# Kernel optimization log

Measured on AMD Instinct MI355X. Metric: run time of the kernel, lower is better.

## Reference

```python
import jax, jax.numpy as jnp
import numpy as np

N = 50000   # nodes
E = 800000  # edges (avg degree 16)
D = 96      # input feature dim
U = 96      # units (== D, so no dense_i projection)


def _glorot(key, fan_in, fan_out):
    limit = np.sqrt(6.0 / (fan_in + fan_out)).astype(np.float32)
    return jax.random.uniform(key, (fan_in, fan_out), jnp.float32, -limit, limit)


def setup_inputs() -> dict:
    key = jax.random.key(0)
    ks = jax.random.split(key, 8)
    X = jax.random.normal(ks[0], (N, D), jnp.float32)
    row = jax.random.randint(ks[1], (E,), 0, N, jnp.int32)   # destination nodes
    col = jax.random.randint(ks[2], (E,), 0, N, jnp.int32)   # source nodes
    a_vals = jax.random.uniform(ks[3], (E,), jnp.float32)    # adjacency values
    return {
        "X": X,
        "a_vals": a_vals,
        "Wn": _glorot(ks[4], D, U), "bn": jnp.zeros((U,), jnp.float32),
        "Wgi": _glorot(ks[5], D, U), "bgi": jnp.zeros((U,), jnp.float32),
        "Wgn": _glorot(ks[6], U, U), "bgn": jnp.zeros((U,), jnp.float32),
        "row": row, "col": col,
    }


def reference(X, a_vals, Wn, bn, Wgi, bgi, Wgn, bgn, row, col):
    # new_X = dense_n(X); new_X = A @ new_X  (SpMM via gather + segment_sum)
    newX = X @ Wn + bn                       # [N, U]
    msgs = a_vals[:, None] * newX[col]       # [E, U]
    agg = jax.ops.segment_sum(msgs, row, num_segments=N)  # [N, U]
    # gate = sigmoid(dense_gate_i(X) + dense_gate_n(agg))
    gate = jax.nn.sigmoid(X @ Wgi + bgi + agg @ Wgn + bgn)
    # units == inp_dim -> no dense_i; gated residual combine
    return agg * gate + X * (1.0 - gate)
```

## Files before the change

### kernel.cpp

```cpp
#include <hip/hip_runtime.h>
#include <math.h>


#define DU 96
#define DU4 24
#define NSUB 64
#define NGRP 8
#define HMAX 6656

typedef unsigned int uint;
typedef unsigned short ushort;
typedef __attribute__((ext_vector_type(8))) short short8;
typedef __attribute__((ext_vector_type(4))) float f32x4;

__device__ inline uint bf16r(float x) {
  uint u = __float_as_uint(x);
  return (u + 0x7FFFu + ((u >> 16) & 1u)) >> 16;
}

__global__ __launch_bounds__(256) void k_fuse1(
    const float* __restrict__ X, const float* __restrict__ Wn,
    const float* __restrict__ bn, const float* __restrict__ Wgi,
    const float* __restrict__ Wgn, const int* __restrict__ row,
    ushort* __restrict__ Xb, ushort* __restrict__ newXb,
    ushort* __restrict__ WTgi, ushort* __restrict__ WTgn,
    int* __restrict__ pc, int N, int E, int ntile) {
  __shared__ __align__(16) char smem[31744];
  ushort* WL = (ushort*)smem;
  typedef ushort XsRow[104];
  XsRow* Xs = (XsRow*)(smem + 18432);
  const int tid = threadIdx.x;
  const int lane = tid & 63, w = tid >> 6;
  const int m = lane & 15, q = lane >> 4;

  if ((int)blockIdx.x < ntile) {
    if (blockIdx.x == 0) {
      for (int i = tid; i < DU * DU; i += 256) {
        int n = i / DU, k = i % DU;
        WTgi[i] = (ushort)bf16r(Wgi[k * DU + n]);
      }
    } else if (blockIdx.x == 1) {
      for (int i = tid; i < DU * DU; i += 256) {
        int n = i / DU, k = i % DU;
        WTgn[i] = (ushort)bf16r(Wgn[k * DU + n]);
      }
    }
    for (int idx = tid; idx < 9216; idx += 256) {
      int j = idx & 7, ln = (idx >> 3) & 63, tk = idx >> 9;
      int ks = tk / 6, t = tk % 6;
      int k = ks * 32 + (ln >> 4) * 8 + j;
      int n = t * 16 + (ln & 15);
      WL[idx] = (ushort)bf16r(Wn[k * DU + n]);
    }
    const int row0 = blockIdx.x * 64;
    for (int i = tid; i < 64 * 48; i += 256) {
      int r = i / 48, cu = i % 48;
      int gr = row0 + r;
      uint packed = 0;
      if (gr < N) {
        float2 v = ((const float2*)X)[(size_t)gr * 48 + cu];
        packed = bf16r(v.x) | (bf16r(v.y) << 16);
        ((uint*)Xb)[(size_t)gr * 48 + cu] = packed;
      }
      *(uint*)&Xs[r][cu * 2] = packed;
    }
    __syncthreads();

    f32x4 acc[6];
#pragma unroll
    for (int t = 0; t < 6; ++t) acc[t] = (f32x4){0.f, 0.f, 0.f, 0.f};
#pragma unroll
    for (int ks = 0; ks < 3; ++ks) {
      short8 af = *(const short8*)&Xs[w * 16 + m][ks * 32 + q * 8];
#pragma unroll
      for (int t = 0; t < 6; ++t) {
        short8 bf = *(const short8*)&WL[((ks * 6 + t) * 64 + lane) * 8];
        acc[t] = __builtin_amdgcn_mfma_f32_16x16x32_bf16(af, bf, acc[t], 0, 0, 0);
      }
    }
    __syncthreads();
#pragma unroll
    for (int t = 0; t < 6; ++t) {
      int c = t * 16 + m;
      float bb = bn[c];
#pragma unroll
      for (int i = 0; i < 4; ++i)
        Xs[w * 16 + q * 4 + i][c] = (ushort)bf16r(acc[t][i] + bb);
    }
    __syncthreads();
    for (int i = tid; i < 64 * 48; i += 256) {
      int r = i / 48, cu = i % 48;
      int gr = row0 + r;
      if (gr < N) ((uint*)newXb)[(size_t)gr * 48 + cu] = *(uint*)&Xs[r][cu * 2];
    }
  } else {
    int* hist = (int*)smem;
    const int hb = (int)blockIdx.x - ntile;
    const int g = (int)(blockIdx.x & 7);
    const int sub = hb >> 3;
    const int d0 = (int)((long long)N * g >> 3);
    const int d1 = (int)((long long)N * (g + 1) >> 3);
    const int hs = d1 - d0;
    for (int j = tid; j < hs; j += 256) hist[j] = 0;
    __syncthreads();
    const int e0 = (int)(((long long)E * sub) >> 6);
    const int e1 = (int)(((long long)E * (sub + 1)) >> 6);
    int i = e0 + tid;
    for (; i + 768 < e1; i += 1024) {
      int a0 = row[i], a1 = row[i + 256], a2 = row[i + 512], a3 = row[i + 768];
      if (a0 >= d0 && a0 < d1) atomicAdd(&hist[a0 - d0], 1);
      if (a1 >= d0 && a1 < d1) atomicAdd(&hist[a1 - d0], 1);
      if (a2 >= d0 && a2 < d1) atomicAdd(&hist[a2 - d0], 1);
      if (a3 >= d0 && a3 < d1) atomicAdd(&hist[a3 - d0], 1);
    }
    for (; i < e1; i += 256) {
      int d = row[i];
      if (d >= d0 && d < d1) atomicAdd(&hist[d - d0], 1);
    }
    __syncthreads();
    for (int j = tid; j < hs; j += 256) pc[(size_t)sub * N + d0 + j] = hist[j];
  }
}

__global__ __launch_bounds__(256) void k_colsum(const int* __restrict__ pc,
                                                int* __restrict__ psub, int N) {
  int d = blockIdx.x * 256 + threadIdx.x;
  if (d >= N) return;
  int run = 0;
#pragma unroll 8
  for (int s = 0; s < NSUB; ++s) {
    int v = pc[(size_t)s * N + d];
    psub[(size_t)s * N + d] = run;
    run += v;
  }
}

__global__ __launch_bounds__(1024) void k_scan(const int* __restrict__ pc,
                                               const int* __restrict__ psub,
                                               int* __restrict__ off, int N) {
  __shared__ int ws[16];
  __shared__ int carry_s;
  const int* pcL = pc + (size_t)(NSUB - 1) * N;
  const int* psL = psub + (size_t)(NSUB - 1) * N;
  const int tid = threadIdx.x;
  const int lane = tid & 63, wid = tid >> 6;
  if (tid == 0) carry_s = 0;
  __syncthreads();
  const int PT = 8;
  const int CH = 1024 * PT;
  for (int base = 0; base < N; base += CH) {
    int idx = base + tid * PT;
    int tot[PT];
    int s = 0;
    if (idx < N) {
      int4 a0 = ((const int4*)(pcL + idx))[0];
      int4 a1 = ((const int4*)(pcL + idx))[1];
      int4 b0 = ((const int4*)(psL + idx))[0];
      int4 b1 = ((const int4*)(psL + idx))[1];
      tot[0] = a0.x + b0.x; tot[1] = a0.y + b0.y;
      tot[2] = a0.z + b0.z; tot[3] = a0.w + b0.w;
      tot[4] = a1.x + b1.x; tot[5] = a1.y + b1.y;
      tot[6] = a1.z + b1.z; tot[7] = a1.w + b1.w;
#pragma unroll
      for (int j = 0; j < PT; ++j) s += tot[j];
    } else {
#pragma unroll
      for (int j = 0; j < PT; ++j) tot[j] = 0;
    }
    int incl = s;
#pragma unroll
    for (int d = 1; d < 64; d <<= 1) {
      int t = __shfl_up(incl, d, 64);
      if (lane >= d) incl += t;
    }
    if (lane == 63) ws[wid] = incl;
    __syncthreads();
    int carry = carry_s;
    int wexcl = 0;
#pragma unroll
    for (int k = 0; k < 16; ++k)
      if (k < wid) wexcl += ws[k];
    int running = carry + wexcl + (incl - s);
    if (idx < N) {
      int4 o1, o2;
      o1.x = running; running += tot[0];
      o1.y = running; running += tot[1];
      o1.z = running; running += tot[2];
      o1.w = running; running += tot[3];
      o2.x = running; running += tot[4];
      o2.y = running; running += tot[5];
      o2.z = running; running += tot[6];
      o2.w = running; running += tot[7];
      ((int4*)(off + idx))[0] = o1;
      ((int4*)(off + idx))[1] = o2;
    }
    __syncthreads();
    if (tid == 0) {
      int t16 = 0;
#pragma unroll
      for (int k = 0; k < 16; ++k) t16 += ws[k];
      carry_s += t16;
    }
    __syncthreads();
  }
  if (tid == 0) off[N] = carry_s;
}

__global__ __launch_bounds__(256) void k_scatter(const int* __restrict__ row,
                                                 const int* __restrict__ col,
                                                 const float* __restrict__ a_vals,
                                                 const int* __restrict__ off,
                                                 const int* __restrict__ psub,
                                                 int2* __restrict__ ec,
                                                 int N, int E) {
  __shared__ int cur[HMAX];
  const int g = (int)(blockIdx.x & 7);
  const int sub = (int)(blockIdx.x >> 3);
  const int d0 = (int)((long long)N * g >> 3);
  const int d1 = (int)((long long)N * (g + 1) >> 3);
  const int hs = d1 - d0;
  for (int j = threadIdx.x; j < hs; j += 256)
    cur[j] = off[d0 + j] + psub[(size_t)sub * N + d0 + j];
  __syncthreads();
  const int e0 = (int)(((long long)E * sub) >> 6);
  const int e1 = (int)(((long long)E * (sub + 1)) >> 6);
  int i = e0 + (int)threadIdx.x;
  for (; i + 768 < e1; i += 1024) {
    int a0 = row[i], a1 = row[i + 256], a2 = row[i + 512], a3 = row[i + 768];
    if (a0 >= d0 && a0 < d1) {
      int s = atomicAdd(&cur[a0 - d0], 1);
      ec[s] = make_int2(col[i], __float_as_int(a_vals[i]));
    }
    if (a1 >= d0 && a1 < d1) {
      int s = atomicAdd(&cur[a1 - d0], 1);
      ec[s] = make_int2(col[i + 256], __float_as_int(a_vals[i + 256]));
    }
    if (a2 >= d0 && a2 < d1) {
      int s = atomicAdd(&cur[a2 - d0], 1);
      ec[s] = make_int2(col[i + 512], __float_as_int(a_vals[i + 512]));
    }
    if (a3 >= d0 && a3 < d1) {
      int s = atomicAdd(&cur[a3 - d0], 1);
      ec[s] = make_int2(col[i + 768], __float_as_int(a_vals[i + 768]));
    }
  }
  for (; i < e1; i += 256) {
    int d = row[i];
    if (d >= d0 && d < d1) {
      int s = atomicAdd(&cur[d - d0], 1);
      ec[s] = make_int2(col[i], __float_as_int(a_vals[i]));
    }
  }
}

__global__ __launch_bounds__(256) void k_agg(const ushort* __restrict__ newXb,
                                             const int* __restrict__ off,
                                             const int2* __restrict__ ec,
                                             ushort* __restrict__ aggb, int N) {
  int i = blockIdx.x * 256 + threadIdx.x;
  int r = i / 12;
  int c = i % 12;
  if (r >= N) return;
  int o0 = off[r];
  int e1 = off[r + 1] - o0;
  const int2* ep = ec + o0;
  float accA[8], accB[8];
#pragma unroll
  for (int k = 0; k < 8; ++k) { accA[k] = 0.f; accB[k] = 0.f; }
  int e = 0;
  for (; e + 4 <= e1; e += 4) {
    int2 p0 = ep[e + 0];
    int2 p1 = ep[e + 1];
    int2 p2 = ep[e + 2];
    int2 p3 = ep[e + 3];
    uint4 v0 = *(const uint4*)(newXb + (size_t)p0.x * DU + c * 8);
    uint4 v1 = *(const uint4*)(newXb + (size_t)p1.x * DU + c * 8);
    uint4 v2 = *(const uint4*)(newXb + (size_t)p2.x * DU + c * 8);
    uint4 v3 = *(const uint4*)(newXb + (size_t)p3.x * DU + c * 8);
    float a0 = __int_as_float(p0.y), a1 = __int_as_float(p1.y);
    float a2 = __int_as_float(p2.y), a3 = __int_as_float(p3.y);
    accA[0] = fmaf(a0, __uint_as_float(v0.x << 16), accA[0]);
    accA[1] = fmaf(a0, __uint_as_float(v0.x & 0xFFFF0000u), accA[1]);
    accA[2] = fmaf(a0, __uint_as_float(v0.y << 16), accA[2]);
    accA[3] = fmaf(a0, __uint_as_float(v0.y & 0xFFFF0000u), accA[3]);
    accA[4] = fmaf(a0, __uint_as_float(v0.z << 16), accA[4]);
    accA[5] = fmaf(a0, __uint_as_float(v0.z & 0xFFFF0000u), accA[5]);
    accA[6] = fmaf(a0, __uint_as_float(v0.w << 16), accA[6]);
    accA[7] = fmaf(a0, __uint_as_float(v0.w & 0xFFFF0000u), accA[7]);
    accB[0] = fmaf(a1, __uint_as_float(v1.x << 16), accB[0]);
    accB[1] = fmaf(a1, __uint_as_float(v1.x & 0xFFFF0000u), accB[1]);
    accB[2] = fmaf(a1, __uint_as_float(v1.y << 16), accB[2]);
    accB[3] = fmaf(a1, __uint_as_float(v1.y & 0xFFFF0000u), accB[3]);
    accB[4] = fmaf(a1, __uint_as_float(v1.z << 16), accB[4]);
    accB[5] = fmaf(a1, __uint_as_float(v1.z & 0xFFFF0000u), accB[5]);
    accB[6] = fmaf(a1, __uint_as_float(v1.w << 16), accB[6]);
    accB[7] = fmaf(a1, __uint_as_float(v1.w & 0xFFFF0000u), accB[7]);
    accA[0] = fmaf(a2, __uint_as_float(v2.x << 16), accA[0]);
    accA[1] = fmaf(a2, __uint_as_float(v2.x & 0xFFFF0000u), accA[1]);
    accA[2] = fmaf(a2, __uint_as_float(v2.y << 16), accA[2]);
    accA[3] = fmaf(a2, __uint_as_float(v2.y & 0xFFFF0000u), accA[3]);
    accA[4] = fmaf(a2, __uint_as_float(v2.z << 16), accA[4]);
    accA[5] = fmaf(a2, __uint_as_float(v2.z & 0xFFFF0000u), accA[5]);
    accA[6] = fmaf(a2, __uint_as_float(v2.w << 16), accA[6]);
    accA[7] = fmaf(a2, __uint_as_float(v2.w & 0xFFFF0000u), accA[7]);
    accB[0] = fmaf(a3, __uint_as_float(v3.x << 16), accB[0]);
    accB[1] = fmaf(a3, __uint_as_float(v3.x & 0xFFFF0000u), accB[1]);
    accB[2] = fmaf(a3, __uint_as_float(v3.y << 16), accB[2]);
    accB[3] = fmaf(a3, __uint_as_float(v3.y & 0xFFFF0000u), accB[3]);
    accB[4] = fmaf(a3, __uint_as_float(v3.z << 16), accB[4]);
    accB[5] = fmaf(a3, __uint_as_float(v3.z & 0xFFFF0000u), accB[5]);
    accB[6] = fmaf(a3, __uint_as_float(v3.w << 16), accB[6]);
    accB[7] = fmaf(a3, __uint_as_float(v3.w & 0xFFFF0000u), accB[7]);
  }
  for (; e < e1; ++e) {
    int2 p = ep[e];
    uint4 v = *(const uint4*)(newXb + (size_t)p.x * DU + c * 8);
    float a = __int_as_float(p.y);
    accA[0] = fmaf(a, __uint_as_float(v.x << 16), accA[0]);
    accA[1] = fmaf(a, __uint_as_float(v.x & 0xFFFF0000u), accA[1]);
    accA[2] = fmaf(a, __uint_as_float(v.y << 16), accA[2]);
    accA[3] = fmaf(a, __uint_as_float(v.y & 0xFFFF0000u), accA[3]);
    accA[4] = fmaf(a, __uint_as_float(v.z << 16), accA[4]);
    accA[5] = fmaf(a, __uint_as_float(v.z & 0xFFFF0000u), accA[5]);
    accA[6] = fmaf(a, __uint_as_float(v.w << 16), accA[6]);
    accA[7] = fmaf(a, __uint_as_float(v.w & 0xFFFF0000u), accA[7]);
  }
#pragma unroll
  for (int k = 0; k < 8; ++k) accA[k] += accB[k];
  uint4 o;
  o.x = bf16r(accA[0]) | (bf16r(accA[1]) << 16);
  o.y = bf16r(accA[2]) | (bf16r(accA[3]) << 16);
  o.z = bf16r(accA[4]) | (bf16r(accA[5]) << 16);
  o.w = bf16r(accA[6]) | (bf16r(accA[7]) << 16);
  *(uint4*)(aggb + (size_t)r * DU + c * 8) = o;
}

__global__ __launch_bounds__(256) void k_gateM(const ushort* __restrict__ Xb,
                                               const ushort* __restrict__ aggb,
                                               const ushort* __restrict__ WTgi,
                                               const ushort* __restrict__ WTgn,
                                               const float* __restrict__ bgi,
                                               const float* __restrict__ bgn,
                                               const float* __restrict__ X,
                                               float* __restrict__ Out, int N) {
  __shared__ float Gs[64][100];
  const int tid = threadIdx.x;
  const int lane = tid & 63, w = tid >> 6;
  const int m = lane & 15, q = lane >> 4;
  const int row0 = blockIdx.x * 64;
  int ar = row0 + w * 16 + m;
  if (ar > N - 1) ar = N - 1;

  f32x4 acc[6];
#pragma unroll
  for (int t = 0; t < 6; ++t) acc[t] = (f32x4){0.f, 0.f, 0.f, 0.f};

#pragma unroll
  for (int ks = 0; ks < 3; ++ks) {
    short8 af = *(const short8*)(Xb + (size_t)ar * DU + ks * 32 + q * 8);
#pragma unroll
    for (int t = 0; t < 6; ++t) {
      short8 bf = *(const short8*)(WTgi + (size_t)(t * 16 + m) * DU + ks * 32 + q * 8);
      acc[t] = __builtin_amdgcn_mfma_f32_16x16x32_bf16(af, bf, acc[t], 0, 0, 0);
    }
  }
#pragma unroll
  for (int ks = 0; ks < 3; ++ks) {
    short8 af = *(const short8*)(aggb + (size_t)ar * DU + ks * 32 + q * 8);
#pragma unroll
    for (int t = 0; t < 6; ++t) {
      short8 bf = *(const short8*)(WTgn + (size_t)(t * 16 + m) * DU + ks * 32 + q * 8);
      acc[t] = __builtin_amdgcn_mfma_f32_16x16x32_bf16(af, bf, acc[t], 0, 0, 0);
    }
  }

#pragma unroll
  for (int t = 0; t < 6; ++t) {
    int c = t * 16 + m;
    float bb = bgi[c] + bgn[c];
#pragma unroll
    for (int i = 0; i < 4; ++i) {
      float z = acc[t][i] + bb;
      Gs[w * 16 + q * 4 + i][c] = 1.f / (1.f + __expf(-z));
    }
  }
  __syncthreads();

  for (int j = tid; j < 64 * DU4; j += 256) {
    int r = j / DU4, c = j % DU4;
    int gr = row0 + r;
    if (gr < N) {
      float4 xv = ((const float4*)X)[(size_t)gr * DU4 + c];
      uint2 av = ((const uint2*)aggb)[(size_t)gr * DU4 + c];
      float a0 = __uint_as_float(av.x << 16);
      float a1 = __uint_as_float(av.x & 0xFFFF0000u);
      float a2 = __uint_as_float(av.y << 16);
      float a3 = __uint_as_float(av.y & 0xFFFF0000u);
      const float* gp = &Gs[r][c * 4];
      float4 o;
      o.x = xv.x + gp[0] * (a0 - xv.x);
      o.y = xv.y + gp[1] * (a1 - xv.y);
      o.z = xv.z + gp[2] * (a2 - xv.z);
      o.w = xv.w + gp[3] * (a3 - xv.w);
      ((float4*)Out)[(size_t)gr * DU4 + c] = o;
    }
  }
}

extern "C" void kernel_launch(void* const* d_in, const int* in_sizes, int n_in,
                              void* d_out, int out_size, void* d_ws, size_t ws_size,
                              hipStream_t stream) {
  const float* X      = (const float*)d_in[0];
  const float* a_vals = (const float*)d_in[1];
  const float* Wn     = (const float*)d_in[2];
  const float* bn     = (const float*)d_in[3];
  const float* Wgi    = (const float*)d_in[4];
  const float* bgi    = (const float*)d_in[5];
  const float* Wgn    = (const float*)d_in[6];
  const float* bgn    = (const float*)d_in[7];
  const int*   row    = (const int*)d_in[8];
  const int*   col    = (const int*)d_in[9];
  float* out = (float*)d_out;

  const int N = in_sizes[0] / DU;
  const int E = in_sizes[1];
  const int ntile = (N + 63) / 64;
  const int G1 = ntile + NSUB * NGRP;

  int2*   ec    = (int2*)d_ws;
  ushort* Xb    = (ushort*)(ec + (size_t)E);
  ushort* newXb = Xb + (size_t)N * DU;
  ushort* aggb  = newXb + (size_t)N * DU;
  ushort* WTgi  = aggb + (size_t)N * DU;
  ushort* WTgn  = WTgi + DU * DU;
  int*    off   = (int*)(WTgn + DU * DU);
  int*    pc    = off + ((N + 4) & ~3);
  int*    psub  = pc + (size_t)NSUB * N;

  k_fuse1  <<<G1, 256, 0, stream>>>(X, Wn, bn, Wgi, Wgn, row,
                                    Xb, newXb, WTgi, WTgn, pc, N, E, ntile);
  k_colsum <<<(N + 255) / 256, 256, 0, stream>>>(pc, psub, N);
  k_scan   <<<1, 1024, 0, stream>>>(pc, psub, off, N);
  k_scatter<<<NSUB * NGRP, 256, 0, stream>>>(row, col, a_vals, off, psub, ec, N, E);
  k_agg    <<<((size_t)N * 12 + 255) / 256, 256, 0, stream>>>(newXb, off, ec, aggb, N);
  k_gateM  <<<ntile, 256, 0, stream>>>(Xb, aggb, WTgi, WTgn, bgi, bgn, X, out, N);
}
```

Measured before the change: 202.0 us.

## Narrow partial counts to 16-bit, unroll edge loops, XCD-grouped aggregation

Per-subchunk histogram counts and their prefix sums are stored as 16-bit values instead of 32-bit. This halves the traffic of the count, colsum and scan stages, and colsum now handles two nodes per thread with packed loads. The histogram and scatter edge loops are unrolled to eight loads, and the aggregation gets an eight-edge unrolled path. Aggregation blocks are also remapped so that blockIdx&7 selects a contiguous node range, which likely keeps off/ec accesses local to each XCD's L2. The 16-bit counts assume per-node degree below 65536, and the packed loads assume N is even.

```diff
diff --git a/kernel.cpp b/kernel.cpp
--- a/kernel.cpp
+++ b/kernel.cpp
@@ -24,7 +24,7 @@
     const float* __restrict__ Wgn, const int* __restrict__ row,
     ushort* __restrict__ Xb, ushort* __restrict__ newXb,
     ushort* __restrict__ WTgi, ushort* __restrict__ WTgn,
-    int* __restrict__ pc, int N, int E, int ntile) {
+    ushort* __restrict__ pc, int N, int E, int ntile) {
   __shared__ __align__(16) char smem[31744];
   ushort* WL = (ushort*)smem;
   typedef ushort XsRow[104];
@@ -106,42 +106,48 @@
     const int e0 = (int)(((long long)E * sub) >> 6);
     const int e1 = (int)(((long long)E * (sub + 1)) >> 6);
     int i = e0 + tid;
-    for (; i + 768 < e1; i += 1024) {
+    for (; i + 1792 < e1; i += 2048) {
       int a0 = row[i], a1 = row[i + 256], a2 = row[i + 512], a3 = row[i + 768];
+      int a4 = row[i + 1024], a5 = row[i + 1280], a6 = row[i + 1536], a7 = row[i + 1792];
       if (a0 >= d0 && a0 < d1) atomicAdd(&hist[a0 - d0], 1);
       if (a1 >= d0 && a1 < d1) atomicAdd(&hist[a1 - d0], 1);
       if (a2 >= d0 && a2 < d1) atomicAdd(&hist[a2 - d0], 1);
       if (a3 >= d0 && a3 < d1) atomicAdd(&hist[a3 - d0], 1);
+      if (a4 >= d0 && a4 < d1) atomicAdd(&hist[a4 - d0], 1);
+      if (a5 >= d0 && a5 < d1) atomicAdd(&hist[a5 - d0], 1);
+      if (a6 >= d0 && a6 < d1) atomicAdd(&hist[a6 - d0], 1);
+      if (a7 >= d0 && a7 < d1) atomicAdd(&hist[a7 - d0], 1);
     }
     for (; i < e1; i += 256) {
       int d = row[i];
       if (d >= d0 && d < d1) atomicAdd(&hist[d - d0], 1);
     }
     __syncthreads();
-    for (int j = tid; j < hs; j += 256) pc[(size_t)sub * N + d0 + j] = hist[j];
-  }
-}
-
-__global__ __launch_bounds__(256) void k_colsum(const int* __restrict__ pc,
-                                                int* __restrict__ psub, int N) {
-  int d = blockIdx.x * 256 + threadIdx.x;
-  if (d >= N) return;
-  int run = 0;
+    for (int j = tid; j < hs; j += 256) pc[(size_t)sub * N + d0 + j] = (ushort)hist[j];
+  }
+}
+
+__global__ __launch_bounds__(256) void k_colsum(const ushort* __restrict__ pc,
+                                                ushort* __restrict__ psub, int N) {
+  int d2 = (blockIdx.x * 256 + threadIdx.x) * 2;
+  if (d2 >= N) return;
+  int runLo = 0, runHi = 0;
 #pragma unroll 8
   for (int s = 0; s < NSUB; ++s) {
-    int v = pc[(size_t)s * N + d];
-    psub[(size_t)s * N + d] = run;
-    run += v;
-  }
-}
-
-__global__ __launch_bounds__(1024) void k_scan(const int* __restrict__ pc,
-                                               const int* __restrict__ psub,
+    uint v = *(const uint*)(pc + (size_t)s * N + d2);
+    *(uint*)(psub + (size_t)s * N + d2) = (uint)runLo | ((uint)runHi << 16);
+    runLo += (int)(v & 0xFFFFu);
+    runHi += (int)(v >> 16);
+  }
+}
+
+__global__ __launch_bounds__(1024) void k_scan(const ushort* __restrict__ pc,
+                                               const ushort* __restrict__ psub,
                                                int* __restrict__ off, int N) {
   __shared__ int ws[16];
   __shared__ int carry_s;
-  const int* pcL = pc + (size_t)(NSUB - 1) * N;
-  const int* psL = psub + (size_t)(NSUB - 1) * N;
+  const ushort* pcL = pc + (size_t)(NSUB - 1) * N;
+  const ushort* psL = psub + (size_t)(NSUB - 1) * N;
   const int tid = threadIdx.x;
   const int lane = tid & 63, wid = tid >> 6;
   if (tid == 0) carry_s = 0;
@@ -153,14 +159,16 @@
     int tot[PT];
     int s = 0;
     if (idx < N) {
-      int4 a0 = ((const int4*)(pcL + idx))[0];
-      int4 a1 = ((const int4*)(pcL + idx))[1];
-      int4 b0 = ((const int4*)(psL + idx))[0];
-      int4 b1 = ((const int4*)(psL + idx))[1];
-      tot[0] = a0.x + b0.x; tot[1] = a0.y + b0.y;
-      tot[2] = a0.z + b0.z; tot[3] = a0.w + b0.w;
-      tot[4] = a1.x + b1.x; tot[5] = a1.y + b1.y;
-      tot[6] = a1.z + b1.z; tot[7] = a1.w + b1.w;
+      uint4 a = *(const uint4*)(pcL + idx);
+      uint4 b = *(const uint4*)(psL + idx);
+      tot[0] = (int)(a.x & 0xFFFFu) + (int)(b.x & 0xFFFFu);
+      tot[1] = (int)(a.x >> 16) + (int)(b.x >> 16);
+      tot[2] = (int)(a.y & 0xFFFFu) + (int)(b.y & 0xFFFFu);
+      tot[3] = (int)(a.y >> 16) + (int)(b.y >> 16);
+      tot[4] = (int)(a.z & 0xFFFFu) + (int)(b.z & 0xFFFFu);
+      tot[5] = (int)(a.z >> 16) + (int)(b.z >> 16);
+      tot[6] = (int)(a.w & 0xFFFFu) + (int)(b.w & 0xFFFFu);
+      tot[7] = (int)(a.w >> 16) + (int)(b.w >> 16);
 #pragma unroll
       for (int j = 0; j < PT; ++j) s += tot[j];
     } else {
@@ -210,7 +218,7 @@
                                                  const int* __restrict__ col,
                                                  const float* __restrict__ a_vals,
                                                  const int* __restrict__ off,
-                                                 const int* __restrict__ psub,
+                                                 const ushort* __restrict__ psub,
                                                  int2* __restrict__ ec,
                                                  int N, int E) {
   __shared__ int cur[HMAX];
@@ -220,13 +228,14 @@
   const int d1 = (int)((long long)N * (g + 1) >> 3);
   const int hs = d1 - d0;
   for (int j = threadIdx.x; j < hs; j += 256)
-    cur[j] = off[d0 + j] + psub[(size_t)sub * N + d0 + j];
+    cur[j] = off[d0 + j] + (int)psub[(size_t)sub * N + d0 + j];
   __syncthreads();
   const int e0 = (int)(((long long)E * sub) >> 6);
   const int e1 = (int)(((long long)E * (sub + 1)) >> 6);
   int i = e0 + (int)threadIdx.x;
-  for (; i + 768 < e1; i += 1024) {
+  for (; i + 1792 < e1; i += 2048) {
     int a0 = row[i], a1 = row[i + 256], a2 = row[i + 512], a3 = row[i + 768];
+    int a4 = row[i + 1024], a5 = row[i + 1280], a6 = row[i + 1536], a7 = row[i + 1792];
     if (a0 >= d0 && a0 < d1) {
       int s = atomicAdd(&cur[a0 - d0], 1);
       ec[s] = make_int2(col[i], __float_as_int(a_vals[i]));
@@ -242,6 +251,22 @@
     if (a3 >= d0 && a3 < d1) {
       int s = atomicAdd(&cur[a3 - d0], 1);
       ec[s] = make_int2(col[i + 768], __float_as_int(a_vals[i + 768]));
+    }
+    if (a4 >= d0 && a4 < d1) {
+      int s = atomicAdd(&cur[a4 - d0], 1);
+      ec[s] = make_int2(col[i + 1024], __float_as_int(a_vals[i + 1024]));
+    }
+    if (a5 >= d0 && a5 < d1) {
+      int s = atomicAdd(&cur[a5 - d0], 1);
+      ec[s] = make_int2(col[i + 1280], __float_as_int(a_vals[i + 1280]));
+    }
+    if (a6 >= d0 && a6 < d1) {
+      int s = atomicAdd(&cur[a6 - d0], 1);
+      ec[s] = make_int2(col[i + 1536], __float_as_int(a_vals[i + 1536]));
+    }
+    if (a7 >= d0 && a7 < d1) {
+      int s = atomicAdd(&cur[a7 - d0], 1);
+      ec[s] = make_int2(col[i + 1792], __float_as_int(a_vals[i + 1792]));
     }
   }
   for (; i < e1; i += 256) {
@@ -257,10 +282,14 @@
                                              const int* __restrict__ off,
                                              const int2* __restrict__ ec,
                                              ushort* __restrict__ aggb, int N) {
-  int i = blockIdx.x * 256 + threadIdx.x;
-  int r = i / 12;
+  const int g = (int)(blockIdx.x & 7);
+  const int b2 = (int)(blockIdx.x >> 3);
+  const int d0 = (int)((long long)N * g >> 3);
+  const int ntask = ((int)((long long)N * (g + 1) >> 3) - d0) * 12;
+  int i = b2 * 256 + threadIdx.x;
+  if (i >= ntask) return;
+  int r = d0 + i / 12;
   int c = i % 12;
-  if (r >= N) return;
   int o0 = off[r];
   int e1 = off[r + 1] - o0;
   const int2* ep = ec + o0;
@@ -268,6 +297,45 @@
 #pragma unroll
   for (int k = 0; k < 8; ++k) { accA[k] = 0.f; accB[k] = 0.f; }
   int e = 0;
+#define GCN_FMA8(ACC, V, A)                                      \
+  ACC[0] = fmaf(A, __uint_as_float(V.x << 16), ACC[0]);          \
+  ACC[1] = fmaf(A, __uint_as_float(V.x & 0xFFFF0000u), ACC[1]);  \
+  ACC[2] = fmaf(A, __uint_as_float(V.y << 16), ACC[2]);          \
+  ACC[3] = fmaf(A, __uint_as_float(V.y & 0xFFFF0000u), ACC[3]);  \
+  ACC[4] = fmaf(A, __uint_as_float(V.z << 16), ACC[4]);          \
+  ACC[5] = fmaf(A, __uint_as_float(V.z & 0xFFFF0000u), ACC[5]);  \
+  ACC[6] = fmaf(A, __uint_as_float(V.w << 16), ACC[6]);          \
+  ACC[7] = fmaf(A, __uint_as_float(V.w & 0xFFFF0000u), ACC[7])
+  for (; e + 8 <= e1; e += 8) {
+    int2 p0 = ep[e + 0];
+    int2 p1 = ep[e + 1];
+    int2 p2 = ep[e + 2];
+    int2 p3 = ep[e + 3];
+    int2 p4 = ep[e + 4];
+    int2 p5 = ep[e + 5];
+    int2 p6 = ep[e + 6];
+    int2 p7 = ep[e + 7];
+    uint4 v0 = *(const uint4*)(newXb + (size_t)p0.x * DU + c * 8);
+    uint4 v1 = *(const uint4*)(newXb + (size_t)p1.x * DU + c * 8);
+    uint4 v2 = *(const uint4*)(newXb + (size_t)p2.x * DU + c * 8);
+    uint4 v3 = *(const uint4*)(newXb + (size_t)p3.x * DU + c * 8);
+    uint4 v4 = *(const uint4*)(newXb + (size_t)p4.x * DU + c * 8);
+    uint4 v5 = *(const uint4*)(newXb + (size_t)p5.x * DU + c * 8);
+    uint4 v6 = *(const uint4*)(newXb + (size_t)p6.x * DU + c * 8);
+    uint4 v7 = *(const uint4*)(newXb + (size_t)p7.x * DU + c * 8);
+    float a0 = __int_as_float(p0.y), a1 = __int_as_float(p1.y);
+    float a2 = __int_as_float(p2.y), a3 = __int_as_float(p3.y);
+    float a4 = __int_as_float(p4.y), a5 = __int_as_float(p5.y);
+    float a6 = __int_as_float(p6.y), a7 = __int_as_float(p7.y);
+    GCN_FMA8(accA, v0, a0);
+    GCN_FMA8(accB, v1, a1);
+    GCN_FMA8(accA, v2, a2);
+    GCN_FMA8(accB, v3, a3);
+    GCN_FMA8(accA, v4, a4);
+    GCN_FMA8(accB, v5, a5);
+    GCN_FMA8(accA, v6, a6);
+    GCN_FMA8(accB, v7, a7);
+  }
   for (; e + 4 <= e1; e += 4) {
     int2 p0 = ep[e + 0];
     int2 p1 = ep[e + 1];
@@ -279,52 +347,18 @@
     uint4 v3 = *(const uint4*)(newXb + (size_t)p3.x * DU + c * 8);
     float a0 = __int_as_float(p0.y), a1 = __int_as_float(p1.y);
     float a2 = __int_as_float(p2.y), a3 = __int_as_float(p3.y);
-    accA[0] = fmaf(a0, __uint_as_float(v0.x << 16), accA[0]);
-    accA[1] = fmaf(a0, __uint_as_float(v0.x & 0xFFFF0000u), accA[1]);
-    accA[2] = fmaf(a0, __uint_as_float(v0.y << 16), accA[2]);
-    accA[3] = fmaf(a0, __uint_as_float(v0.y & 0xFFFF0000u), accA[3]);
-    accA[4] = fmaf(a0, __uint_as_float(v0.z << 16), accA[4]);
-    accA[5] = fmaf(a0, __uint_as_float(v0.z & 0xFFFF0000u), accA[5]);
-    accA[6] = fmaf(a0, __uint_as_float(v0.w << 16), accA[6]);
-    accA[7] = fmaf(a0, __uint_as_float(v0.w & 0xFFFF0000u), accA[7]);
-    accB[0] = fmaf(a1, __uint_as_float(v1.x << 16), accB[0]);
-    accB[1] = fmaf(a1, __uint_as_float(v1.x & 0xFFFF0000u), accB[1]);
-    accB[2] = fmaf(a1, __uint_as_float(v1.y << 16), accB[2]);
-    accB[3] = fmaf(a1, __uint_as_float(v1.y & 0xFFFF0000u), accB[3]);
-    accB[4] = fmaf(a1, __uint_as_float(v1.z << 16), accB[4]);
-    accB[5] = fmaf(a1, __uint_as_float(v1.z & 0xFFFF0000u), accB[5]);
-    accB[6] = fmaf(a1, __uint_as_float(v1.w << 16), accB[6]);
-    accB[7] = fmaf(a1, __uint_as_float(v1.w & 0xFFFF0000u), accB[7]);
-    accA[0] = fmaf(a2, __uint_as_float(v2.x << 16), accA[0]);
-    accA[1] = fmaf(a2, __uint_as_float(v2.x & 0xFFFF0000u), accA[1]);
-    accA[2] = fmaf(a2, __uint_as_float(v2.y << 16), accA[2]);
-    accA[3] = fmaf(a2, __uint_as_float(v2.y & 0xFFFF0000u), accA[3]);
-    accA[4] = fmaf(a2, __uint_as_float(v2.z << 16), accA[4]);
-    accA[5] = fmaf(a2, __uint_as_float(v2.z & 0xFFFF0000u), accA[5]);
-    accA[6] = fmaf(a2, __uint_as_float(v2.w << 16), accA[6]);
-    accA[7] = fmaf(a2, __uint_as_float(v2.w & 0xFFFF0000u), accA[7]);
-    accB[0] = fmaf(a3, __uint_as_float(v3.x << 16), accB[0]);
-    accB[1] = fmaf(a3, __uint_as_float(v3.x & 0xFFFF0000u), accB[1]);
-    accB[2] = fmaf(a3, __uint_as_float(v3.y << 16), accB[2]);
-    accB[3] = fmaf(a3, __uint_as_float(v3.y & 0xFFFF0000u), accB[3]);
-    accB[4] = fmaf(a3, __uint_as_float(v3.z << 16), accB[4]);
-    accB[5] = fmaf(a3, __uint_as_float(v3.z & 0xFFFF0000u), accB[5]);
-    accB[6] = fmaf(a3, __uint_as_float(v3.w << 16), accB[6]);
-    accB[7] = fmaf(a3, __uint_as_float(v3.w & 0xFFFF0000u), accB[7]);
+    GCN_FMA8(accA, v0, a0);
+    GCN_FMA8(accB, v1, a1);
+    GCN_FMA8(accA, v2, a2);
+    GCN_FMA8(accB, v3, a3);
   }
   for (; e < e1; ++e) {
     int2 p = ep[e];
     uint4 v = *(const uint4*)(newXb + (size_t)p.x * DU + c * 8);
     float a = __int_as_float(p.y);
-    accA[0] = fmaf(a, __uint_as_float(v.x << 16), accA[0]);
-    accA[1] = fmaf(a, __uint_as_float(v.x & 0xFFFF0000u), accA[1]);
-    accA[2] = fmaf(a, __uint_as_float(v.y << 16), accA[2]);
-    accA[3] = fmaf(a, __uint_as_float(v.y & 0xFFFF0000u), accA[3]);
-    accA[4] = fmaf(a, __uint_as_float(v.z << 16), accA[4]);
-    accA[5] = fmaf(a, __uint_as_float(v.z & 0xFFFF0000u), accA[5]);
-    accA[6] = fmaf(a, __uint_as_float(v.w << 16), accA[6]);
-    accA[7] = fmaf(a, __uint_as_float(v.w & 0xFFFF0000u), accA[7]);
-  }
+    GCN_FMA8(accA, v, a);
+  }
+#undef GCN_FMA8
 #pragma unroll
   for (int k = 0; k < 8; ++k) accA[k] += accB[k];
   uint4 o;
@@ -434,14 +468,16 @@
   ushort* WTgi  = aggb + (size_t)N * DU;
   ushort* WTgn  = WTgi + DU * DU;
   int*    off   = (int*)(WTgn + DU * DU);
-  int*    pc    = off + ((N + 4) & ~3);
-  int*    psub  = pc + (size_t)NSUB * N;
+  ushort* pc    = (ushort*)(off + ((N + 4) & ~3));
+  ushort* psub  = pc + (size_t)NSUB * N;
+
+  const int aggBPG = (int)(((long long)N * 12 / 8 + 255) / 256);
 
   k_fuse1  <<<G1, 256, 0, stream>>>(X, Wn, bn, Wgi, Wgn, row,
                                     Xb, newXb, WTgi, WTgn, pc, N, E, ntile);
-  k_colsum <<<(N + 255) / 256, 256, 0, stream>>>(pc, psub, N);
+  k_colsum <<<(N / 2 + 255) / 256, 256, 0, stream>>>(pc, psub, N);
   k_scan   <<<1, 1024, 0, stream>>>(pc, psub, off, N);
   k_scatter<<<NSUB * NGRP, 256, 0, stream>>>(row, col, a_vals, off, psub, ec, N, E);
-  k_agg    <<<((size_t)N * 12 + 255) / 256, 256, 0, stream>>>(newXb, off, ec, aggb, N);
+  k_agg    <<<aggBPG * NGRP, 256, 0, stream>>>(newXb, off, ec, aggb, N);
   k_gateM  <<<ntile, 256, 0, stream>>>(Xb, aggb, WTgi, WTgn, bgi, bgn, X, out, N);
 }
```

Result: faster. 196.6 us (-2.6%).
